# Kernel optimization log

Measured on AMD Instinct MI355X. Metric: run time of the kernel, lower is better.

Reference implementation:

```python
import jax, jax.numpy as jnp
import numpy as np

BS = 128          # block size for fp8 block-scaled quantization
FP8_MAX = 448.0   # max normal value of float8_e4m3fn


def _weight_quant(w):
    """Quantize weight [O, I] with per-(128x128)-block scales, DeepSeek-V3 style.
    Returns (w_q stored as fp32 holding fp8-representable values, scale [O/BS, I/BS])."""
    O, I = w.shape
    wb = w.reshape(O // BS, BS, I // BS, BS)
    amax = jnp.max(jnp.abs(wb), axis=(1, 3))
    scale = jnp.where(amax == 0, 1.0, amax / FP8_MAX)
    q = (wb / scale[:, None, :, None]).astype(jnp.float8_e4m3fn).astype(jnp.float32)
    return q.reshape(O, I), scale


def _act_qdq(x):
    """act_quant + dequant: per-128-block (last dim) fp8 quantization of activations."""
    T, D = x.shape
    xb = x.reshape(T, D // BS, BS)
    amax = jnp.max(jnp.abs(xb), axis=-1, keepdims=True)
    scale = jnp.where(amax == 0, 1.0, amax / FP8_MAX)
    q = (xb / scale).astype(jnp.float8_e4m3fn).astype(jnp.float32)
    return (q * scale).reshape(T, D)


def _dequant_w(wq, ws):
    O, I = wq.shape
    return (wq.reshape(O // BS, BS, I // BS, BS) * ws[:, None, :, None]).reshape(O, I)


def _linear_fp8(x, wq, ws):
    # fp8_gemm with per-block scales == dequantized GEMM in fp32 accumulate
    return _act_qdq(x) @ _dequant_w(wq, ws).T


def setup_inputs() -> dict:
    T, DIM, INTER = 2048, 4096, 11008
    key = jax.random.key(0)
    kx, k1, k2, k3 = jax.random.split(key, 4)
    x = jax.random.normal(kx, (T, DIM), dtype=jnp.float32)
    w1 = jax.random.normal(k1, (INTER, DIM), dtype=jnp.float32) * 0.02
    w2 = jax.random.normal(k2, (DIM, INTER), dtype=jnp.float32) * 0.02
    w3 = jax.random.normal(k3, (INTER, DIM), dtype=jnp.float32) * 0.02
    w1_q, w1_s = _weight_quant(w1)
    w2_q, w2_s = _weight_quant(w2)
    w3_q, w3_s = _weight_quant(w3)
    return {"x": x, "w1_q": w1_q, "w1_s": w1_s, "w2_q": w2_q, "w2_s": w2_s,
            "w3_q": w3_q, "w3_s": w3_s}


def reference(x, w1_q, w1_s, w2_q, w2_s, w3_q, w3_s):
    # SwiGLU: w2( silu(w1(x)) * w3(x) ), each linear is fp8 block-scaled GEMM
    h = jax.nn.silu(_linear_fp8(x, w1_q, w1_s)) * _linear_fp8(x, w3_q, w3_s)
    return _linear_fp8(h, w2_q, w2_s)
```

## Files before the change

### kernel.cpp

```cpp
#include <hip/hip_runtime.h>
#include <hip/hip_fp8.h>

#define T_DIM 2048
#define D_DIM 4096
#define I_DIM 11008

typedef int v8i __attribute__((ext_vector_type(8)));
typedef float v4f __attribute__((ext_vector_type(4)));

__device__ inline void async_copy16(const void* g, void* l) {
  __builtin_amdgcn_global_load_lds((const __attribute__((address_space(1))) void*)g,
                                   (__attribute__((address_space(3))) void*)l, 16, 0, 0);
}

__global__ void quant_x_kernel(const float* __restrict__ X, unsigned char* __restrict__ Q,
                               float* __restrict__ St, const int T, const int D) {
  const int wave = (blockIdx.x << 2) + (threadIdx.x >> 6);
  const int lane = threadIdx.x & 63;
  const int nb = D >> 7;
  const int t = wave / nb;
  const int kb = wave - t * nb;
  const size_t base = (size_t)t * D + ((size_t)kb << 7);
  const float2 v = ((const float2*)(X + base))[lane];
  float a = fmaxf(fabsf(v.x), fabsf(v.y));
#pragma unroll
  for (int off = 32; off > 0; off >>= 1) a = fmaxf(a, __shfl_xor(a, off));
  const float scale = (a == 0.f) ? 1.f : (a / 448.f);
  unsigned short pk = (unsigned short)__builtin_amdgcn_cvt_pk_fp8_f32(v.x / scale, v.y / scale, 0, false);
  ((unsigned short*)(Q + base))[lane] = pk;
  if (lane == 0) St[(size_t)kb * T + t] = scale;
}

__global__ void silu_mul_quant_kernel(const float* __restrict__ H1, const float* __restrict__ H3,
                                      unsigned char* __restrict__ Q, float* __restrict__ St,
                                      const int T, const int D) {
  const int wave = (blockIdx.x << 2) + (threadIdx.x >> 6);
  const int lane = threadIdx.x & 63;
  const int nb = D >> 7;
  const int t = wave / nb;
  const int kb = wave - t * nb;
  const size_t base = (size_t)t * D + ((size_t)kb << 7);
  const float2 v1 = ((const float2*)(H1 + base))[lane];
  const float2 v3 = ((const float2*)(H3 + base))[lane];
  const float hx = (v1.x / (1.f + __expf(-v1.x))) * v3.x;
  const float hy = (v1.y / (1.f + __expf(-v1.y))) * v3.y;
  float a = fmaxf(fabsf(hx), fabsf(hy));
#pragma unroll
  for (int off = 32; off > 0; off >>= 1) a = fmaxf(a, __shfl_xor(a, off));
  const float scale = (a == 0.f) ? 1.f : (a / 448.f);
  unsigned short pk = (unsigned short)__builtin_amdgcn_cvt_pk_fp8_f32(hx / scale, hy / scale, 0, false);
  ((unsigned short*)(Q + base))[lane] = pk;
  if (lane == 0) St[(size_t)kb * T + t] = scale;
}

__global__ void convert_fp8_kernel(const float4* __restrict__ W, unsigned int* __restrict__ Q,
                                   const int n4) {
  const int i = blockIdx.x * 256 + threadIdx.x;
  if (i >= n4) return;
  const float4 f = W[i];
  int r = __builtin_amdgcn_cvt_pk_fp8_f32(f.x, f.y, 0, false);
  r = __builtin_amdgcn_cvt_pk_fp8_f32(f.z, f.w, r, true);
  Q[i] = (unsigned int)r;
}

__device__ inline void stage_tiles(const unsigned char* gA, const unsigned char* gB,
                                   unsigned char* lA, unsigned char* lB,
                                   size_t koff, const int K) {
#pragma unroll
  for (int t = 0; t < 4; ++t)
    async_copy16(gA + (size_t)(t * 8) * K + koff, lA + (t << 10));
#pragma unroll
  for (int t = 0; t < 4; ++t)
    async_copy16(gB + (size_t)(t * 8) * K + koff, lB + (t << 10));
}

__device__ inline void load_scales(const float* __restrict__ sArow, const float* __restrict__ sBrow,
                                   int kb, int M, float4 sa[4], float& sb) {
  const float4* sap = (const float4*)(sArow + (size_t)kb * M);
#pragma unroll
  for (int i = 0; i < 4; ++i) sa[i] = sap[i * 4];
  sb = sBrow[kb];
}

__device__ inline void compute_step(const unsigned char* __restrict__ Asb,
                                    const unsigned char* __restrict__ Bsb,
                                    int wm, int wn, int row16, int quad,
                                    const float4 sa[4], float sb, v4f acc[4][4]) {
  v4f zero = {0.f, 0.f, 0.f, 0.f};
  v8i a[4], b[4];
#pragma unroll
  for (int i = 0; i < 4; ++i)
    a[i] = *(const v8i*)&Asb[((wm + (i << 4) + row16) << 7) + (quad << 5)];
#pragma unroll
  for (int j = 0; j < 4; ++j)
    b[j] = *(const v8i*)&Bsb[((wn + (j << 4) + row16) << 7) + (quad << 5)];

#pragma unroll
  for (int i = 0; i < 4; ++i) {
    v4f cs;
    cs.x = sa[i].x * sb; cs.y = sa[i].y * sb;
    cs.z = sa[i].z * sb; cs.w = sa[i].w * sb;
#pragma unroll
    for (int j = 0; j < 4; ++j) {
      v4f p = __builtin_amdgcn_mfma_scale_f32_16x16x128_f8f6f4(
          a[i], b[j], zero, 0, 0, 0, 0x7f7f7f7f, 0, 0x7f7f7f7f);
      acc[i][j] += cs * p;
    }
  }
}

template <int NKB>
__global__ __launch_bounds__(256, 2) void gemm_fp8_bs(
    const unsigned char* __restrict__ A, const float* __restrict__ sAt,
    const unsigned char* __restrict__ B, const float* __restrict__ sB,
    float* __restrict__ C, const int M, const int N) {
  const int K = NKB << 7;
  __shared__ unsigned char As[2][128 * 128];
  __shared__ unsigned char Bs[2][128 * 128];

  const int tid = threadIdx.x;
  const int lane = tid & 63;
  const int w = tid >> 6;
  const int wm = (w >> 1) << 6;
  const int wn = (w & 1) << 6;
  const int row16 = lane & 15;
  const int quad = lane >> 4;
  const int m0 = blockIdx.x << 7;
  const int n0 = blockIdx.y << 7;

  const int srow = (w << 5) + (lane >> 3);
  const int scol = (lane & 7) << 4;
  const unsigned char* gA = A + (size_t)(m0 + srow) * K + scol;
  const unsigned char* gB = B + (size_t)(n0 + srow) * K + scol;
  unsigned char* lA0 = &As[0][w << 12];
  unsigned char* lB0 = &Bs[0][w << 12];
  unsigned char* lA1 = &As[1][w << 12];
  unsigned char* lB1 = &Bs[1][w << 12];

  v4f acc[4][4];
#pragma unroll
  for (int i = 0; i < 4; ++i)
#pragma unroll
    for (int j = 0; j < 4; ++j) acc[i][j] = (v4f){0.f, 0.f, 0.f, 0.f};

  const float* sArow = sAt + m0 + wm + (quad << 2);
  const float* sBrow = sB + (size_t)(n0 >> 7) * NKB;

  float4 sa_c[4], sa_n[4];
  float sb_c, sb_n;

  load_scales(sArow, sBrow, 0, M, sa_c, sb_c);
  stage_tiles(gA, gB, lA0, lB0, 0, K);
  __syncthreads();

  for (int kb = 0; kb < NKB; kb += 2) {
    stage_tiles(gA, gB, lA1, lB1, (size_t)(kb + 1) << 7, K);
    load_scales(sArow, sBrow, kb + 1, M, sa_n, sb_n);
    compute_step(&As[0][0], &Bs[0][0], wm, wn, row16, quad, sa_c, sb_c, acc);
    __syncthreads();

    const int kb2 = (kb + 2 < NKB) ? kb + 2 : 0;
    if (kb + 2 < NKB) stage_tiles(gA, gB, lA0, lB0, (size_t)(kb + 2) << 7, K);
    load_scales(sArow, sBrow, kb2, M, sa_c, sb_c);
    compute_step(&As[1][0], &Bs[1][0], wm, wn, row16, quad, sa_n, sb_n, acc);
    __syncthreads();
  }

#pragma unroll
  for (int i = 0; i < 4; ++i) {
    const size_t rbase = (size_t)(m0 + wm + (i << 4) + (quad << 2));
#pragma unroll
    for (int r = 0; r < 4; ++r) {
      float* crow = C + (rbase + r) * N + n0 + wn + row16;
#pragma unroll
      for (int j = 0; j < 4; ++j) crow[j << 4] = acc[i][j][r];
    }
  }
}

extern "C" void kernel_launch(void* const* d_in, const int* in_sizes, int n_in,
                              void* d_out, int out_size, void* d_ws, size_t ws_size,
                              hipStream_t stream) {
  const float* x   = (const float*)d_in[0];
  const float* w1q = (const float*)d_in[1];
  const float* w1s = (const float*)d_in[2];
  const float* w2q = (const float*)d_in[3];
  const float* w2s = (const float*)d_in[4];
  const float* w3q = (const float*)d_in[5];
  const float* w3s = (const float*)d_in[6];

  unsigned char* ws = (unsigned char*)d_ws;
  const size_t SZ_QX = (size_t)T_DIM * D_DIM;
  const size_t SZ_W  = (size_t)I_DIM * D_DIM;
  const size_t SZ_QH = (size_t)T_DIM * I_DIM;
  const size_t SZ_SX = (size_t)(D_DIM / 128) * T_DIM * 4;
  const size_t SZ_SH = (size_t)(I_DIM / 128) * T_DIM * 4;
  const size_t SZ_H  = (size_t)T_DIM * I_DIM * 4;

  unsigned char* qx   = ws;             ws += SZ_QX;
  unsigned char* w1q8 = ws;             ws += SZ_W;
  unsigned char* w3q8 = ws;             ws += SZ_W;
  unsigned char* w2q8 = ws;             ws += SZ_W;
  unsigned char* qh   = ws;             ws += SZ_QH;
  float* sxt = (float*)ws;              ws += SZ_SX;
  float* sht = (float*)ws;              ws += SZ_SH;
  float* h1  = (float*)ws;              ws += SZ_H;
  float* h3  = (float*)ws;              ws += SZ_H;

  quant_x_kernel<<<(T_DIM * (D_DIM / 128)) / 4, 256, 0, stream>>>(x, qx, sxt, T_DIM, D_DIM);

  const int n4w = (int)(SZ_W / 4);
  convert_fp8_kernel<<<(n4w + 255) / 256, 256, 0, stream>>>((const float4*)w1q, (unsigned int*)w1q8, n4w);
  convert_fp8_kernel<<<(n4w + 255) / 256, 256, 0, stream>>>((const float4*)w3q, (unsigned int*)w3q8, n4w);
  convert_fp8_kernel<<<(n4w + 255) / 256, 256, 0, stream>>>((const float4*)w2q, (unsigned int*)w2q8, n4w);

  dim3 g13(T_DIM / 128, I_DIM / 128);
  gemm_fp8_bs<D_DIM / 128><<<g13, 256, 0, stream>>>(qx, sxt, w1q8, w1s, h1, T_DIM, I_DIM);
  gemm_fp8_bs<D_DIM / 128><<<g13, 256, 0, stream>>>(qx, sxt, w3q8, w3s, h3, T_DIM, I_DIM);

  silu_mul_quant_kernel<<<(T_DIM * (I_DIM / 128)) / 4, 256, 0, stream>>>(h1, h3, qh, sht, T_DIM, I_DIM);

  dim3 g2(T_DIM / 128, D_DIM / 128);
  gemm_fp8_bs<I_DIM / 128><<<g2, 256, 0, stream>>>(qh, sht, w2q8, w2s, (float*)d_out, T_DIM, D_DIM);

  (void)in_sizes; (void)n_in; (void)out_size; (void)ws_size;
}
```

Measured before the change: 1.031 ms.

## Replace async LDS double buffer with register-staged padded single-buffer GEMM pipeline

The GEMM drops direct global-to-LDS async copies with two LDS buffers. Instead it loads the next k-block into registers while computing the current one, and uses a single LDS buffer padded to a 144-byte row stride to avoid bank conflicts on fragment reads. The quant and silu kernels now process two 128-blocks per wave with float4 loads and a reciprocal multiply, and the weight convert kernel becomes grid-stride with a fixed grid. Each k-step needs two barriers and more registers, and the LDS footprint is halved.

```diff
diff --git a/kernel.cpp b/kernel.cpp
--- a/kernel.cpp
+++ b/kernel.cpp
@@ -7,28 +7,27 @@
 
 typedef int v8i __attribute__((ext_vector_type(8)));
 typedef float v4f __attribute__((ext_vector_type(4)));
-
-__device__ inline void async_copy16(const void* g, void* l) {
-  __builtin_amdgcn_global_load_lds((const __attribute__((address_space(1))) void*)g,
-                                   (__attribute__((address_space(3))) void*)l, 16, 0, 0);
-}
 
 __global__ void quant_x_kernel(const float* __restrict__ X, unsigned char* __restrict__ Q,
                                float* __restrict__ St, const int T, const int D) {
   const int wave = (blockIdx.x << 2) + (threadIdx.x >> 6);
   const int lane = threadIdx.x & 63;
+  const int qb = (wave << 1) + (lane >> 5);
+  const int l = lane & 31;
   const int nb = D >> 7;
-  const int t = wave / nb;
-  const int kb = wave - t * nb;
+  const int t = qb / nb;
+  const int kb = qb - t * nb;
   const size_t base = (size_t)t * D + ((size_t)kb << 7);
-  const float2 v = ((const float2*)(X + base))[lane];
-  float a = fmaxf(fabsf(v.x), fabsf(v.y));
-#pragma unroll
-  for (int off = 32; off > 0; off >>= 1) a = fmaxf(a, __shfl_xor(a, off));
+  const float4 v = ((const float4*)(X + base))[l];
+  float a = fmaxf(fmaxf(fabsf(v.x), fabsf(v.y)), fmaxf(fabsf(v.z), fabsf(v.w)));
+#pragma unroll
+  for (int off = 16; off > 0; off >>= 1) a = fmaxf(a, __shfl_xor(a, off));
   const float scale = (a == 0.f) ? 1.f : (a / 448.f);
-  unsigned short pk = (unsigned short)__builtin_amdgcn_cvt_pk_fp8_f32(v.x / scale, v.y / scale, 0, false);
-  ((unsigned short*)(Q + base))[lane] = pk;
-  if (lane == 0) St[(size_t)kb * T + t] = scale;
+  const float inv = 1.f / scale;
+  int r = __builtin_amdgcn_cvt_pk_fp8_f32(v.x * inv, v.y * inv, 0, false);
+  r = __builtin_amdgcn_cvt_pk_fp8_f32(v.z * inv, v.w * inv, r, true);
+  ((unsigned int*)(Q + base))[l] = (unsigned int)r;
+  if (l == 0) St[(size_t)kb * T + t] = scale;
 }
 
 __global__ void silu_mul_quant_kernel(const float* __restrict__ H1, const float* __restrict__ H3,
@@ -36,78 +35,42 @@
                                       const int T, const int D) {
   const int wave = (blockIdx.x << 2) + (threadIdx.x >> 6);
   const int lane = threadIdx.x & 63;
+  const int qb = (wave << 1) + (lane >> 5);
+  const int l = lane & 31;
   const int nb = D >> 7;
-  const int t = wave / nb;
-  const int kb = wave - t * nb;
+  const int t = qb / nb;
+  const int kb = qb - t * nb;
   const size_t base = (size_t)t * D + ((size_t)kb << 7);
-  const float2 v1 = ((const float2*)(H1 + base))[lane];
-  const float2 v3 = ((const float2*)(H3 + base))[lane];
-  const float hx = (v1.x / (1.f + __expf(-v1.x))) * v3.x;
-  const float hy = (v1.y / (1.f + __expf(-v1.y))) * v3.y;
-  float a = fmaxf(fabsf(hx), fabsf(hy));
-#pragma unroll
-  for (int off = 32; off > 0; off >>= 1) a = fmaxf(a, __shfl_xor(a, off));
+  const float4 v1 = ((const float4*)(H1 + base))[l];
+  const float4 v3 = ((const float4*)(H3 + base))[l];
+  float4 h;
+  h.x = (v1.x / (1.f + __expf(-v1.x))) * v3.x;
+  h.y = (v1.y / (1.f + __expf(-v1.y))) * v3.y;
+  h.z = (v1.z / (1.f + __expf(-v1.z))) * v3.z;
+  h.w = (v1.w / (1.f + __expf(-v1.w))) * v3.w;
+  float a = fmaxf(fmaxf(fabsf(h.x), fabsf(h.y)), fmaxf(fabsf(h.z), fabsf(h.w)));
+#pragma unroll
+  for (int off = 16; off > 0; off >>= 1) a = fmaxf(a, __shfl_xor(a, off));
   const float scale = (a == 0.f) ? 1.f : (a / 448.f);
-  unsigned short pk = (unsigned short)__builtin_amdgcn_cvt_pk_fp8_f32(hx / scale, hy / scale, 0, false);
-  ((unsigned short*)(Q + base))[lane] = pk;
-  if (lane == 0) St[(size_t)kb * T + t] = scale;
+  const float inv = 1.f / scale;
+  int r = __builtin_amdgcn_cvt_pk_fp8_f32(h.x * inv, h.y * inv, 0, false);
+  r = __builtin_amdgcn_cvt_pk_fp8_f32(h.z * inv, h.w * inv, r, true);
+  ((unsigned int*)(Q + base))[l] = (unsigned int)r;
+  if (l == 0) St[(size_t)kb * T + t] = scale;
 }
 
 __global__ void convert_fp8_kernel(const float4* __restrict__ W, unsigned int* __restrict__ Q,
                                    const int n4) {
-  const int i = blockIdx.x * 256 + threadIdx.x;
-  if (i >= n4) return;
-  const float4 f = W[i];
-  int r = __builtin_amdgcn_cvt_pk_fp8_f32(f.x, f.y, 0, false);
-  r = __builtin_amdgcn_cvt_pk_fp8_f32(f.z, f.w, r, true);
-  Q[i] = (unsigned int)r;
-}
-
-__device__ inline void stage_tiles(const unsigned char* gA, const unsigned char* gB,
-                                   unsigned char* lA, unsigned char* lB,
-                                   size_t koff, const int K) {
-#pragma unroll
-  for (int t = 0; t < 4; ++t)
-    async_copy16(gA + (size_t)(t * 8) * K + koff, lA + (t << 10));
-#pragma unroll
-  for (int t = 0; t < 4; ++t)
-    async_copy16(gB + (size_t)(t * 8) * K + koff, lB + (t << 10));
-}
-
-__device__ inline void load_scales(const float* __restrict__ sArow, const float* __restrict__ sBrow,
-                                   int kb, int M, float4 sa[4], float& sb) {
-  const float4* sap = (const float4*)(sArow + (size_t)kb * M);
-#pragma unroll
-  for (int i = 0; i < 4; ++i) sa[i] = sap[i * 4];
-  sb = sBrow[kb];
-}
-
-__device__ inline void compute_step(const unsigned char* __restrict__ Asb,
-                                    const unsigned char* __restrict__ Bsb,
-                                    int wm, int wn, int row16, int quad,
-                                    const float4 sa[4], float sb, v4f acc[4][4]) {
-  v4f zero = {0.f, 0.f, 0.f, 0.f};
-  v8i a[4], b[4];
-#pragma unroll
-  for (int i = 0; i < 4; ++i)
-    a[i] = *(const v8i*)&Asb[((wm + (i << 4) + row16) << 7) + (quad << 5)];
-#pragma unroll
-  for (int j = 0; j < 4; ++j)
-    b[j] = *(const v8i*)&Bsb[((wn + (j << 4) + row16) << 7) + (quad << 5)];
-
-#pragma unroll
-  for (int i = 0; i < 4; ++i) {
-    v4f cs;
-    cs.x = sa[i].x * sb; cs.y = sa[i].y * sb;
-    cs.z = sa[i].z * sb; cs.w = sa[i].w * sb;
-#pragma unroll
-    for (int j = 0; j < 4; ++j) {
-      v4f p = __builtin_amdgcn_mfma_scale_f32_16x16x128_f8f6f4(
-          a[i], b[j], zero, 0, 0, 0, 0x7f7f7f7f, 0, 0x7f7f7f7f);
-      acc[i][j] += cs * p;
-    }
-  }
-}
+  const int stride = gridDim.x * 256;
+  for (int i = blockIdx.x * 256 + threadIdx.x; i < n4; i += stride) {
+    const float4 f = W[i];
+    int r = __builtin_amdgcn_cvt_pk_fp8_f32(f.x, f.y, 0, false);
+    r = __builtin_amdgcn_cvt_pk_fp8_f32(f.z, f.w, r, true);
+    Q[i] = (unsigned int)r;
+  }
+}
+
+#define LSTR 144
 
 template <int NKB>
 __global__ __launch_bounds__(256, 2) void gemm_fp8_bs(
@@ -115,8 +78,8 @@
     const unsigned char* __restrict__ B, const float* __restrict__ sB,
     float* __restrict__ C, const int M, const int N) {
   const int K = NKB << 7;
-  __shared__ unsigned char As[2][128 * 128];
-  __shared__ unsigned char Bs[2][128 * 128];
+  __shared__ unsigned char As[128 * LSTR];
+  __shared__ unsigned char Bs[128 * LSTR];
 
   const int tid = threadIdx.x;
   const int lane = tid & 63;
@@ -132,10 +95,7 @@
   const int scol = (lane & 7) << 4;
   const unsigned char* gA = A + (size_t)(m0 + srow) * K + scol;
   const unsigned char* gB = B + (size_t)(n0 + srow) * K + scol;
-  unsigned char* lA0 = &As[0][w << 12];
-  unsigned char* lB0 = &Bs[0][w << 12];
-  unsigned char* lA1 = &As[1][w << 12];
-  unsigned char* lB1 = &Bs[1][w << 12];
+  const int lofs = srow * LSTR + scol;
 
   v4f acc[4][4];
 #pragma unroll
@@ -146,24 +106,79 @@
   const float* sArow = sAt + m0 + wm + (quad << 2);
   const float* sBrow = sB + (size_t)(n0 >> 7) * NKB;
 
+  int4 ra[4], rb[4];
   float4 sa_c[4], sa_n[4];
   float sb_c, sb_n;
 
-  load_scales(sArow, sBrow, 0, M, sa_c, sb_c);
-  stage_tiles(gA, gB, lA0, lB0, 0, K);
-  __syncthreads();
-
-  for (int kb = 0; kb < NKB; kb += 2) {
-    stage_tiles(gA, gB, lA1, lB1, (size_t)(kb + 1) << 7, K);
-    load_scales(sArow, sBrow, kb + 1, M, sa_n, sb_n);
-    compute_step(&As[0][0], &Bs[0][0], wm, wn, row16, quad, sa_c, sb_c, acc);
+#pragma unroll
+  for (int t = 0; t < 4; ++t) {
+    ra[t] = *(const int4*)(gA + (size_t)(t * 8) * K);
+    rb[t] = *(const int4*)(gB + (size_t)(t * 8) * K);
+  }
+  {
+    const float4* sap = (const float4*)(sArow);
+#pragma unroll
+    for (int i = 0; i < 4; ++i) sa_c[i] = sap[i * 4];
+    sb_c = sBrow[0];
+  }
+
+  for (int kb = 0; kb < NKB; ++kb) {
     __syncthreads();
-
-    const int kb2 = (kb + 2 < NKB) ? kb + 2 : 0;
-    if (kb + 2 < NKB) stage_tiles(gA, gB, lA0, lB0, (size_t)(kb + 2) << 7, K);
-    load_scales(sArow, sBrow, kb2, M, sa_c, sb_c);
-    compute_step(&As[1][0], &Bs[1][0], wm, wn, row16, quad, sa_n, sb_n, acc);
+#pragma unroll
+    for (int t = 0; t < 4; ++t) {
+      *(int4*)(As + lofs + t * 8 * LSTR) = ra[t];
+      *(int4*)(Bs + lofs + t * 8 * LSTR) = rb[t];
+    }
+    const int kn = (kb + 1 < NKB) ? kb + 1 : NKB - 1;
+    {
+      const size_t koff = (size_t)kn << 7;
+#pragma unroll
+      for (int t = 0; t < 4; ++t) {
+        ra[t] = *(const int4*)(gA + (size_t)(t * 8) * K + koff);
+        rb[t] = *(const int4*)(gB + (size_t)(t * 8) * K + koff);
+      }
+      const float4* sap = (const float4*)(sArow + (size_t)kn * M);
+#pragma unroll
+      for (int i = 0; i < 4; ++i) sa_n[i] = sap[i * 4];
+      sb_n = sBrow[kn];
+    }
     __syncthreads();
+
+    v4f zero = {0.f, 0.f, 0.f, 0.f};
+    v8i a[4], b[4];
+#pragma unroll
+    for (int i = 0; i < 4; ++i) {
+      const unsigned char* p = As + (wm + (i << 4) + row16) * LSTR + (quad << 5);
+      union { v8i v; int4 h[2]; } u;
+      u.h[0] = *(const int4*)(p);
+      u.h[1] = *(const int4*)(p + 16);
+      a[i] = u.v;
+    }
+#pragma unroll
+    for (int j = 0; j < 4; ++j) {
+      const unsigned char* p = Bs + (wn + (j << 4) + row16) * LSTR + (quad << 5);
+      union { v8i v; int4 h[2]; } u;
+      u.h[0] = *(const int4*)(p);
+      u.h[1] = *(const int4*)(p + 16);
+      b[j] = u.v;
+    }
+
+#pragma unroll
+    for (int i = 0; i < 4; ++i) {
+      v4f cs;
+      cs.x = sa_c[i].x * sb_c; cs.y = sa_c[i].y * sb_c;
+      cs.z = sa_c[i].z * sb_c; cs.w = sa_c[i].w * sb_c;
+#pragma unroll
+      for (int j = 0; j < 4; ++j) {
+        v4f p = __builtin_amdgcn_mfma_scale_f32_16x16x128_f8f6f4(
+            a[i], b[j], zero, 0, 0, 0, 0x7f7f7f7f, 0, 0x7f7f7f7f);
+        acc[i][j] += cs * p;
+      }
+    }
+
+#pragma unroll
+    for (int i = 0; i < 4; ++i) sa_c[i] = sa_n[i];
+    sb_c = sb_n;
   }
 
 #pragma unroll
@@ -207,18 +222,18 @@
   float* h1  = (float*)ws;              ws += SZ_H;
   float* h3  = (float*)ws;              ws += SZ_H;
 
-  quant_x_kernel<<<(T_DIM * (D_DIM / 128)) / 4, 256, 0, stream>>>(x, qx, sxt, T_DIM, D_DIM);
+  quant_x_kernel<<<(T_DIM * (D_DIM / 128)) / 8, 256, 0, stream>>>(x, qx, sxt, T_DIM, D_DIM);
 
   const int n4w = (int)(SZ_W / 4);
-  convert_fp8_kernel<<<(n4w + 255) / 256, 256, 0, stream>>>((const float4*)w1q, (unsigned int*)w1q8, n4w);
-  convert_fp8_kernel<<<(n4w + 255) / 256, 256, 0, stream>>>((const float4*)w3q, (unsigned int*)w3q8, n4w);
-  convert_fp8_kernel<<<(n4w + 255) / 256, 256, 0, stream>>>((const float4*)w2q, (unsigned int*)w2q8, n4w);
+  convert_fp8_kernel<<<2048, 256, 0, stream>>>((const float4*)w1q, (unsigned int*)w1q8, n4w);
+  convert_fp8_kernel<<<2048, 256, 0, stream>>>((const float4*)w3q, (unsigned int*)w3q8, n4w);
+  convert_fp8_kernel<<<2048, 256, 0, stream>>>((const float4*)w2q, (unsigned int*)w2q8, n4w);
 
   dim3 g13(T_DIM / 128, I_DIM / 128);
   gemm_fp8_bs<D_DIM / 128><<<g13, 256, 0, stream>>>(qx, sxt, w1q8, w1s, h1, T_DIM, I_DIM);
   gemm_fp8_bs<D_DIM / 128><<<g13, 256, 0, stream>>>(qx, sxt, w3q8, w3s, h3, T_DIM, I_DIM);
 
-  silu_mul_quant_kernel<<<(T_DIM * (I_DIM / 128)) / 4, 256, 0, stream>>>(h1, h3, qh, sht, T_DIM, I_DIM);
+  silu_mul_quant_kernel<<<(T_DIM * (I_DIM / 128)) / 8, 256, 0, stream>>>(h1, h3, qh, sht, T_DIM, I_DIM);
 
   dim3 g2(T_DIM / 128, D_DIM / 128);
   gemm_fp8_bs<I_DIM / 128><<<g2, 256, 0, stream>>>(qh, sht, w2q8, w2s, (float*)d_out, T_DIM, D_DIM);
```

Result: slower. 2.043 ms (+98.1%).
